# Kernel tuning notes

Hardware: AMD Instinct MI355X
Metric: run time of the kernel (lower is better)

Reference implementation:

```python
import jax, jax.numpy as jnp
import numpy as np

N_NODES = 100000
N_EDGES = 1600000
IN_DIM = 512
OUT_DIM = 64


def setup_inputs() -> dict:
    key = jax.random.key(0)
    k1, k2, k3 = jax.random.split(key, 3)
    x = jax.random.normal(k1, (N_NODES, IN_DIM), dtype=jnp.float32)
    edge_index = jax.random.randint(k2, (2, N_EDGES), 0, N_NODES, dtype=jnp.int64)
    # Glorot-ish init for the GCNConv linear weight, stored as [in, out]
    W = jax.random.normal(k3, (IN_DIM, OUT_DIM), dtype=jnp.float32) * (1.0 / np.sqrt(IN_DIM))
    b = jnp.zeros((OUT_DIM,), dtype=jnp.float32)
    return {"x": x, "edge_index": edge_index, "W": W, "b": b}


def reference(x, edge_index, W, b):
    N = x.shape[0]
    # --- gcn_norm: add self-loops, symmetric degree normalization ---
    loop = jnp.arange(N, dtype=edge_index.dtype)
    src = jnp.concatenate([edge_index[0], loop])  # message sources
    dst = jnp.concatenate([edge_index[1], loop])  # aggregation targets
    deg = jax.ops.segment_sum(jnp.ones_like(dst, dtype=x.dtype), dst, num_segments=N)
    deg_inv_sqrt = jnp.where(deg > 0, jax.lax.rsqrt(jnp.maximum(deg, 1.0)), 0.0)
    norm = deg_inv_sqrt[src] * deg_inv_sqrt[dst]  # [E+N]
    # --- linear transform then gather-scale-scatter aggregation ---
    h = x @ W                                   # [N, out]
    msg = h[src] * norm[:, None]                # [E+N, out]
    out = jax.ops.segment_sum(msg, dst, num_segments=N) + b
    return jax.nn.log_softmax(out, axis=1)
```

## Files before the change

kernel.cpp:

```cpp
#include <hip/hip_runtime.h>
#include <math.h>

#define N_NODES 100000
#define N_EDGES 1600000
#define IN_DIM 512
#define OUT_DIM 64
#define NB 1024
#define NPB 128
#define CHUNK (N_EDGES / NPB)
#define N_BUCKETS_USED 782
#define N_TILES (N_NODES / 16)
#define GEMM_WAVES 4096

typedef __attribute__((ext_vector_type(8))) short short8;
typedef __attribute__((ext_vector_type(4))) float float4v;

__device__ __forceinline__ unsigned short f2bf(float f) {
    unsigned int u = __float_as_uint(f);
    u += 0x7fffu + ((u >> 16) & 1u);
    return (unsigned short)(u >> 16);
}
__device__ __forceinline__ float bf2f(unsigned short s) {
    return __uint_as_float(((unsigned int)s) << 16);
}
__device__ __forceinline__ float bf2f_lo(unsigned int u) {
    return __uint_as_float(u << 16);
}
__device__ __forceinline__ float bf2f_hi(unsigned int u) {
    return __uint_as_float(u & 0xffff0000u);
}
__device__ __forceinline__ short8 cvt8(float4v lo, float4v hi) {
    union { short8 s8; unsigned short us[8]; } af;
    af.us[0] = f2bf(lo.x); af.us[1] = f2bf(lo.y);
    af.us[2] = f2bf(lo.z); af.us[3] = f2bf(lo.w);
    af.us[4] = f2bf(hi.x); af.us[5] = f2bf(hi.y);
    af.us[6] = f2bf(hi.z); af.us[7] = f2bf(hi.w);
    return af.s8;
}

__global__ __launch_bounds__(256) void k_hist1(const int* __restrict__ dst,
                                               int* __restrict__ blockHist) {
    __shared__ int hist[NB];
    const int t = threadIdx.x, b = blockIdx.x;
    for (int k = t; k < NB; k += 256) hist[k] = 0;
    __syncthreads();
    const int e0 = b * CHUNK;
    for (int i = t; i < CHUNK; i += 256)
        atomicAdd(&hist[dst[e0 + i] >> 7], 1);
    __syncthreads();
    for (int k = t; k < NB; k += 256) blockHist[b * NB + k] = hist[k];
}

__global__ __launch_bounds__(256) void k_offsets(const int* __restrict__ blockHist,
                                                 int* __restrict__ blockStart,
                                                 int* __restrict__ bucketBase) {
    __shared__ int colsum[NB];
    __shared__ int bbase[NB + 1];
    __shared__ int wtot[4];
    const int t = threadIdx.x, lane = t & 63, w = t >> 6;
    for (int k = t; k < NB; k += 256) {
        int s = 0;
        for (int b = 0; b < NPB; ++b) s += blockHist[b * NB + k];
        colsum[k] = s;
    }
    __syncthreads();
    int c0 = colsum[t * 4 + 0], c1 = colsum[t * 4 + 1];
    int c2 = colsum[t * 4 + 2], c3 = colsum[t * 4 + 3];
    int tsum = c0 + c1 + c2 + c3;
    int incl = tsum;
#pragma unroll
    for (int off = 1; off < 64; off <<= 1) {
        int u = __shfl_up(incl, off, 64);
        if (lane >= off) incl += u;
    }
    if (lane == 63) wtot[w] = incl;
    __syncthreads();
    int woff = 0;
#pragma unroll
    for (int k2 = 0; k2 < 4; ++k2) if (k2 < w) woff += wtot[k2];
    int excl = woff + incl - tsum;
    bbase[t * 4 + 0] = excl;
    bbase[t * 4 + 1] = excl + c0;
    bbase[t * 4 + 2] = excl + c0 + c1;
    bbase[t * 4 + 3] = excl + c0 + c1 + c2;
    if (t == 255) bbase[NB] = excl + tsum;
    __syncthreads();
    for (int k = t; k < NB + 1; k += 256) bucketBase[k] = bbase[k];
    for (int k = t; k < NB; k += 256) {
        int run = bbase[k];
        for (int b = 0; b < NPB; ++b) {
            blockStart[b * NB + k] = run;
            run += blockHist[b * NB + k];
        }
    }
}

__global__ __launch_bounds__(256) void k_partition(const int* __restrict__ dst,
                                                   const int* __restrict__ src,
                                                   const int* __restrict__ blockStart,
                                                   int* __restrict__ parts) {
    __shared__ int cursor[NB];
    const int t = threadIdx.x, b = blockIdx.x;
    for (int k = t; k < NB; k += 256) cursor[k] = blockStart[b * NB + k];
    __syncthreads();
    const int e0 = b * CHUNK;
    for (int i = t; i < CHUNK; i += 256) {
        int d = dst[e0 + i];
        int s = src[e0 + i];
        int k = d >> 7;
        int pos = atomicAdd(&cursor[k], 1);
        parts[pos] = ((d & 127) << 17) | s;
    }
}

__global__ __launch_bounds__(256) void k_bucket(const int* __restrict__ parts,
                                                const int* __restrict__ bucketBase,
                                                int* __restrict__ degi,
                                                int* __restrict__ row_ptr,
                                                int* __restrict__ csr) {
    __shared__ int cnt[128];
    __shared__ int cur[128];
    __shared__ int wtot[2];
    const int t = threadIdx.x, k = blockIdx.x;
    const int base = bucketBase[k];
    const int n    = bucketBase[k + 1] - base;
    if (t < 128) cnt[t] = 0;
    __syncthreads();
    for (int i = t; i < n; i += 256)
        atomicAdd(&cnt[parts[base + i] >> 17], 1);
    __syncthreads();
    int incl = 0, v = 0;
    if (t < 128) {
        int lane = t & 63;
        v = cnt[t];
        incl = v;
#pragma unroll
        for (int off = 1; off < 64; off <<= 1) {
            int u = __shfl_up(incl, off, 64);
            if (lane >= off) incl += u;
        }
        if (lane == 63) wtot[t >> 6] = incl;
    }
    __syncthreads();
    if (t < 128) {
        int excl = incl - v + ((t >> 6) ? wtot[0] : 0);
        cur[t] = excl;
        int node = k * 128 + t;
        if (node < N_NODES) {
            degi[node]    = v;
            row_ptr[node] = base + excl;
        }
    }
    __syncthreads();
    for (int i = t; i < n; i += 256) {
        int code = parts[base + i];
        int nl = code >> 17, s = code & 0x1FFFF;
        int pos = atomicAdd(&cur[nl], 1);
        csr[base + pos] = s;
    }
}

__global__ __launch_bounds__(256) void k_wswz(const float* __restrict__ W,
                                              unsigned short* __restrict__ Wswz) {
    int t = blockIdx.x * 256 + threadIdx.x;
    if (t < IN_DIM * OUT_DIM) {
        int k = t >> 6, n = t & 63;
        int kt = k >> 5, kin = k & 31;
        int quad = kin >> 3, j = kin & 7;
        int ct = n >> 4, l16 = n & 15;
        int lane = quad * 16 + l16;
        Wswz[(((kt * 4 + ct) * 64 + lane) * 8) + j] = f2bf(W[t]);
    }
}

__global__ __launch_bounds__(512, 2) void k_gemm(const float* __restrict__ x,
                                              const unsigned short* __restrict__ Wswz,
                                              const int* __restrict__ degi,
                                              unsigned short* __restrict__ h) {
    __shared__ short8 Wlds[64][64];
    const int t = threadIdx.x;
    {
        const float4v* s = (const float4v*)Wswz;
        float4v* d = (float4v*)Wlds;
        for (int i = t; i < 4096; i += 512) d[i] = s[i];
    }
    __syncthreads();

    const int lane = t & 63;
    const int quad = lane >> 4, l16 = lane & 15;
    const int wid = blockIdx.x * 8 + (t >> 6);

    const int t0 = (int)(((long)wid * N_TILES) / GEMM_WAVES);
    const int t1 = (int)(((long)(wid + 1) * N_TILES) / GEMM_WAVES);

    for (int tile = t0; tile < t1; ++tile) {
        const int r0 = tile * 16;
        const float* xrow = x + (size_t)(r0 + l16) * IN_DIM + quad * 8;

        float4v plo[4], phi[4];
#pragma unroll
        for (int kt = 0; kt < 4; ++kt) {
            plo[kt] = *(const float4v*)(xrow + kt * 32);
            phi[kt] = *(const float4v*)(xrow + kt * 32 + 4);
        }
        float4v acc[4] = {{0.f,0.f,0.f,0.f},{0.f,0.f,0.f,0.f},
                          {0.f,0.f,0.f,0.f},{0.f,0.f,0.f,0.f}};

#pragma unroll 1
        for (int kq = 0; kq < 4; ++kq) {
            short8 A[4];
#pragma unroll
            for (int kt = 0; kt < 4; ++kt) A[kt] = cvt8(plo[kt], phi[kt]);
            if (kq < 3) {
#pragma unroll
                for (int kt = 0; kt < 4; ++kt) {
                    plo[kt] = *(const float4v*)(xrow + (kq + 1) * 128 + kt * 32);
                    phi[kt] = *(const float4v*)(xrow + (kq + 1) * 128 + kt * 32 + 4);
                }
            }
#pragma unroll
            for (int kt = 0; kt < 4; ++kt) {
#pragma unroll
                for (int ct = 0; ct < 4; ++ct) {
                    short8 bf = Wlds[(kq * 4 + kt) * 4 + ct][lane];
                    acc[ct] = __builtin_amdgcn_mfma_f32_16x16x32_bf16(A[kt], bf, acc[ct], 0, 0, 0);
                }
            }
        }

#pragma unroll
        for (int reg = 0; reg < 4; ++reg) {
            int orow = r0 + quad * 4 + reg;
            float dinv = rsqrtf((float)(degi[orow] + 1));
#pragma unroll
            for (int ct = 0; ct < 4; ++ct)
                h[(size_t)orow * OUT_DIM + ct * 16 + l16] = f2bf(acc[ct][reg] * dinv);
        }
    }
}

__global__ __launch_bounds__(256) void k_gather(const int* __restrict__ degi,
                                                const int* __restrict__ row_ptr,
                                                const int* __restrict__ csr,
                                                const unsigned short* __restrict__ h,
                                                const float* __restrict__ b,
                                                float* __restrict__ out) {
    int node = blockIdx.x * 4 + (threadIdx.x >> 6);
    int lane = threadIdx.x & 63;
    if (node >= N_NODES) return;
    const int sub = lane >> 4;
    const int c4  = lane & 15;
    int cnt  = __builtin_amdgcn_readfirstlane(degi[node]);
    int base = __builtin_amdgcn_readfirstlane(row_ptr[node]);

    float a0 = 0.f, a1 = 0.f, a2 = 0.f, a3 = 0.f;
    if (sub == 0) {
        uint2 v = *(const uint2*)(h + (size_t)node * OUT_DIM + c4 * 4);
        a0 = bf2f_lo(v.x); a1 = bf2f_hi(v.x);
        a2 = bf2f_lo(v.y); a3 = bf2f_hi(v.y);
    }

    int e = sub;
    for (; e + 4 < cnt; e += 8) {
        int s0 = csr[base + e];
        int s1 = csr[base + e + 4];
        uint2 va = *(const uint2*)(h + (size_t)s0 * OUT_DIM + c4 * 4);
        uint2 vb = *(const uint2*)(h + (size_t)s1 * OUT_DIM + c4 * 4);
        a0 += bf2f_lo(va.x) + bf2f_lo(vb.x);
        a1 += bf2f_hi(va.x) + bf2f_hi(vb.x);
        a2 += bf2f_lo(va.y) + bf2f_lo(vb.y);
        a3 += bf2f_hi(va.y) + bf2f_hi(vb.y);
    }
    if (e < cnt) {
        int s0 = csr[base + e];
        uint2 va = *(const uint2*)(h + (size_t)s0 * OUT_DIM + c4 * 4);
        a0 += bf2f_lo(va.x); a1 += bf2f_hi(va.x);
        a2 += bf2f_lo(va.y); a3 += bf2f_hi(va.y);
    }

    a0 += __shfl_xor(a0, 16, 64); a0 += __shfl_xor(a0, 32, 64);
    a1 += __shfl_xor(a1, 16, 64); a1 += __shfl_xor(a1, 32, 64);
    a2 += __shfl_xor(a2, 16, 64); a2 += __shfl_xor(a2, 32, 64);
    a3 += __shfl_xor(a3, 16, 64); a3 += __shfl_xor(a3, 32, 64);

    float dinv = rsqrtf((float)(cnt + 1));
    const float4v bb = *(const float4v*)(b + c4 * 4);
    float v0 = a0 * dinv + bb.x;
    float v1 = a1 * dinv + bb.y;
    float v2 = a2 * dinv + bb.z;
    float v3 = a3 * dinv + bb.w;

    float m = fmaxf(fmaxf(v0, v1), fmaxf(v2, v3));
#pragma unroll
    for (int off = 1; off < 16; off <<= 1) m = fmaxf(m, __shfl_xor(m, off, 64));
    float s = expf(v0 - m) + expf(v1 - m) + expf(v2 - m) + expf(v3 - m);
#pragma unroll
    for (int off = 1; off < 16; off <<= 1) s += __shfl_xor(s, off, 64);
    float ls = m + logf(s);

    if (sub == 0) {
        float4v r = {v0 - ls, v1 - ls, v2 - ls, v3 - ls};
        *(float4v*)(out + (size_t)node * OUT_DIM + c4 * 4) = r;
    }
}

extern "C" void kernel_launch(void* const* d_in, const int* in_sizes, int n_in,
                              void* d_out, int out_size, void* d_ws, size_t ws_size,
                              hipStream_t stream) {
    const float* x  = (const float*)d_in[0];
    const int*   ei = (const int*)d_in[1];
    const float* W  = (const float*)d_in[2];
    const float* b  = (const float*)d_in[3];
    float* out = (float*)d_out;

    char* ws = (char*)d_ws;
    int*            degi       = (int*)(ws + 0);
    int*            row_ptr    = (int*)(ws + 400000);
    int*            blockHist  = (int*)(ws + 800000);
    int*            blockStart = (int*)(ws + 1324288);
    int*            bucketBase = (int*)(ws + 1848576);
    unsigned short* Wswz       = (unsigned short*)(ws + 1852928);
    unsigned short* h          = (unsigned short*)(ws + 1918464);
    int*            parts      = (int*)(ws + 14718464);
    int*            csr        = (int*)(ws + 21118464);

    const int* src = ei;
    const int* dst = ei + N_EDGES;

    k_hist1    <<<NPB, 256, 0, stream>>>(dst, blockHist);
    k_offsets  <<<1,   256, 0, stream>>>(blockHist, blockStart, bucketBase);
    k_partition<<<NPB, 256, 0, stream>>>(dst, src, blockStart, parts);
    k_bucket   <<<N_BUCKETS_USED, 256, 0, stream>>>(parts, bucketBase, degi, row_ptr, csr);
    k_wswz     <<<(IN_DIM * OUT_DIM + 255) / 256, 256, 0, stream>>>(W, Wswz);
    k_gemm     <<<512, 512, 0, stream>>>(x, Wswz, degi, h);
    k_gather   <<<(N_NODES + 3) / 4, 256, 0, stream>>>(degi, row_ptr, csr, h, b, out);
}
```

Baseline: 455.7 us.

## Assign one 32-row tile per GEMM wave with interleaved dual-tile MFMA pipeline

The GEMM now gives each wave exactly one 32-row tile, made of two 16-row halves, instead of a loop over several 16-row tiles. Each W fragment loaded from LDS is reused for both halves. The x loads are prefetched in 64-column steps, and sched_barriers interleave the two halves so their loads overlap with MFMA work. The grid shrinks to 391 blocks, giving fewer resident waves and less latency hiding from occupancy, while the kernel remains memory-bound on streaming x.

```diff
diff --git a/kernel.cpp b/kernel.cpp
--- a/kernel.cpp
+++ b/kernel.cpp
@@ -9,8 +9,8 @@
 #define NPB 128
 #define CHUNK (N_EDGES / NPB)
 #define N_BUCKETS_USED 782
-#define N_TILES (N_NODES / 16)
-#define GEMM_WAVES 4096
+#define N_TILES32 3125
+#define GEMM_BLOCKS 391
 
 typedef __attribute__((ext_vector_type(8))) short short8;
 typedef __attribute__((ext_vector_type(4))) float float4v;
@@ -188,53 +188,84 @@
 
     const int lane = t & 63;
     const int quad = lane >> 4, l16 = lane & 15;
-    const int wid = blockIdx.x * 8 + (t >> 6);
-
-    const int t0 = (int)(((long)wid * N_TILES) / GEMM_WAVES);
-    const int t1 = (int)(((long)(wid + 1) * N_TILES) / GEMM_WAVES);
-
-    for (int tile = t0; tile < t1; ++tile) {
-        const int r0 = tile * 16;
-        const float* xrow = x + (size_t)(r0 + l16) * IN_DIM + quad * 8;
-
-        float4v plo[4], phi[4];
-#pragma unroll
-        for (int kt = 0; kt < 4; ++kt) {
-            plo[kt] = *(const float4v*)(xrow + kt * 32);
-            phi[kt] = *(const float4v*)(xrow + kt * 32 + 4);
-        }
-        float4v acc[4] = {{0.f,0.f,0.f,0.f},{0.f,0.f,0.f,0.f},
-                          {0.f,0.f,0.f,0.f},{0.f,0.f,0.f,0.f}};
+    const int gw = blockIdx.x * 8 + (t >> 6);
+    if (gw >= N_TILES32) return;
+
+    const int r0 = gw * 32;
+    const float* xA = x + (size_t)(r0 + l16) * IN_DIM + quad * 8;
+    const float* xB = x + (size_t)(r0 + 16 + l16) * IN_DIM + quad * 8;
+
+    float4v aL0 = *(const float4v*)(xA + 0);
+    float4v aH0 = *(const float4v*)(xA + 4);
+    float4v aL1 = *(const float4v*)(xA + 32);
+    float4v aH1 = *(const float4v*)(xA + 36);
+    float4v bL0 = *(const float4v*)(xB + 0);
+    float4v bH0 = *(const float4v*)(xB + 4);
+    float4v bL1 = *(const float4v*)(xB + 32);
+    float4v bH1 = *(const float4v*)(xB + 36);
+
+    float4v accA[4] = {{0.f,0.f,0.f,0.f},{0.f,0.f,0.f,0.f},
+                       {0.f,0.f,0.f,0.f},{0.f,0.f,0.f,0.f}};
+    float4v accB[4] = {{0.f,0.f,0.f,0.f},{0.f,0.f,0.f,0.f},
+                       {0.f,0.f,0.f,0.f},{0.f,0.f,0.f,0.f}};
 
 #pragma unroll 1
-        for (int kq = 0; kq < 4; ++kq) {
-            short8 A[4];
-#pragma unroll
-            for (int kt = 0; kt < 4; ++kt) A[kt] = cvt8(plo[kt], phi[kt]);
-            if (kq < 3) {
-#pragma unroll
-                for (int kt = 0; kt < 4; ++kt) {
-                    plo[kt] = *(const float4v*)(xrow + (kq + 1) * 128 + kt * 32);
-                    phi[kt] = *(const float4v*)(xrow + (kq + 1) * 128 + kt * 32 + 4);
-                }
-            }
-#pragma unroll
-            for (int kt = 0; kt < 4; ++kt) {
-#pragma unroll
-                for (int ct = 0; ct < 4; ++ct) {
-                    short8 bf = Wlds[(kq * 4 + kt) * 4 + ct][lane];
-                    acc[ct] = __builtin_amdgcn_mfma_f32_16x16x32_bf16(A[kt], bf, acc[ct], 0, 0, 0);
-                }
-            }
-        }
-
-#pragma unroll
-        for (int reg = 0; reg < 4; ++reg) {
-            int orow = r0 + quad * 4 + reg;
-            float dinv = rsqrtf((float)(degi[orow] + 1));
-#pragma unroll
-            for (int ct = 0; ct < 4; ++ct)
-                h[(size_t)orow * OUT_DIM + ct * 16 + l16] = f2bf(acc[ct][reg] * dinv);
+    for (int s = 0; s < 8; ++s) {
+        const int kb = s * 64;
+        {
+            short8 A0 = cvt8(aL0, aH0);
+            short8 A1 = cvt8(aL1, aH1);
+            if (s < 7) {
+                aL0 = *(const float4v*)(xA + kb + 64);
+                aH0 = *(const float4v*)(xA + kb + 68);
+                aL1 = *(const float4v*)(xA + kb + 96);
+                aH1 = *(const float4v*)(xA + kb + 100);
+            }
+#pragma unroll
+            for (int ct = 0; ct < 4; ++ct) {
+                short8 w0 = Wlds[(2 * s) * 4 + ct][lane];
+                accA[ct] = __builtin_amdgcn_mfma_f32_16x16x32_bf16(A0, w0, accA[ct], 0, 0, 0);
+            }
+#pragma unroll
+            for (int ct = 0; ct < 4; ++ct) {
+                short8 w1 = Wlds[(2 * s + 1) * 4 + ct][lane];
+                accA[ct] = __builtin_amdgcn_mfma_f32_16x16x32_bf16(A1, w1, accA[ct], 0, 0, 0);
+            }
+        }
+        __builtin_amdgcn_sched_barrier(0);
+        {
+            short8 B0 = cvt8(bL0, bH0);
+            short8 B1 = cvt8(bL1, bH1);
+            if (s < 7) {
+                bL0 = *(const float4v*)(xB + kb + 64);
+                bH0 = *(const float4v*)(xB + kb + 68);
+                bL1 = *(const float4v*)(xB + kb + 96);
+                bH1 = *(const float4v*)(xB + kb + 100);
+            }
+#pragma unroll
+            for (int ct = 0; ct < 4; ++ct) {
+                short8 w0 = Wlds[(2 * s) * 4 + ct][lane];
+                accB[ct] = __builtin_amdgcn_mfma_f32_16x16x32_bf16(B0, w0, accB[ct], 0, 0, 0);
+            }
+#pragma unroll
+            for (int ct = 0; ct < 4; ++ct) {
+                short8 w1 = Wlds[(2 * s + 1) * 4 + ct][lane];
+                accB[ct] = __builtin_amdgcn_mfma_f32_16x16x32_bf16(B1, w1, accB[ct], 0, 0, 0);
+            }
+        }
+        __builtin_amdgcn_sched_barrier(0);
+    }
+
+#pragma unroll
+    for (int reg = 0; reg < 4; ++reg) {
+        int orowA = r0 + quad * 4 + reg;
+        int orowB = orowA + 16;
+        float dA = rsqrtf((float)(degi[orowA] + 1));
+        float dB = rsqrtf((float)(degi[orowB] + 1));
+#pragma unroll
+        for (int ct = 0; ct < 4; ++ct) {
+            h[(size_t)orowA * OUT_DIM + ct * 16 + l16] = f2bf(accA[ct][reg] * dA);
+            h[(size_t)orowB * OUT_DIM + ct * 16 + l16] = f2bf(accB[ct][reg] * dB);
         }
     }
 }
@@ -332,6 +363,6 @@
     k_partition<<<NPB, 256, 0, stream>>>(dst, src, blockStart, parts);
     k_bucket   <<<N_BUCKETS_USED, 256, 0, stream>>>(parts, bucketBase, degi, row_ptr, csr);
     k_wswz     <<<(IN_DIM * OUT_DIM + 255) / 256, 256, 0, stream>>>(W, Wswz);
-    k_gemm     <<<512, 512, 0, stream>>>(x, Wswz, degi, h);
+    k_gemm     <<<GEMM_BLOCKS, 512, 0, stream>>>(x, Wswz, degi, h);
     k_gather   <<<(N_NODES + 3) / 4, 256, 0, stream>>>(degi, row_ptr, csr, h, b, out);
 }
```

New measurement: 458.0 us. No clear change (+0.5%).
